# Kernel optimization log

Hardware: AMD Instinct MI355X
Metric: run time of the kernel (lower is better)

Reference implementation:

```python
import jax, jax.numpy as jnp
import numpy as np

N = 50000      # nodes
E = 800000     # edges (avg degree 16)
F_IN = 128     # num_features
HID = 128      # hidden_channels
C = 40         # num_classes


def setup_inputs() -> dict:
    key = jax.random.key(0)
    ks = jax.random.split(key, 8)
    x = jax.random.normal(ks[0], (N, F_IN), dtype=jnp.float32)
    edge_index = jax.random.randint(ks[1], (2, E), 0, N, dtype=jnp.int64)
    def glorot(k, fan_in, fan_out):
        s = np.sqrt(6.0 / (fan_in + fan_out)).astype(np.float32)
        return jax.random.uniform(k, (fan_in, fan_out), jnp.float32, -s, s)
    return {
        "x": x,
        "W1": glorot(ks[2], F_IN, HID), "b1": jnp.zeros((HID,), jnp.float32),
        "W2": glorot(ks[3], HID, HID),  "b2": jnp.zeros((HID,), jnp.float32),
        "W3": glorot(ks[4], HID, C),   "b3": jnp.zeros((C,), jnp.float32),
        "edge_index": edge_index,
    }


def reference(x, W1, b1, W2, b2, W3, b3, edge_index):
    # GCN with symmetric normalization and self-loops (PyG GCNConv semantics),
    # eval mode (dropout p=0.0), log-softmax output.
    src = edge_index[0]
    dst = edge_index[1]
    loop = jnp.arange(N, dtype=edge_index.dtype)
    src = jnp.concatenate([src, loop])      # [E+N]
    dst = jnp.concatenate([dst, loop])      # [E+N]
    ew = jnp.ones((E + N,), jnp.float32)    # edge_weight=None -> ones
    # deg[i] = sum of incoming edge weights at node i (aggregation index = dst/col)
    deg = jax.ops.segment_sum(ew, dst, num_segments=N)
    dinv = jnp.where(deg > 0, jax.lax.rsqrt(deg), 0.0)
    norm = dinv[src] * ew * dinv[dst]       # [E+N]

    def conv(h, W, b):
        # linear transform first (no bias), then gather->scale->scatter-add, then bias
        m = (h @ W)[src] * norm[:, None]                      # [E+N, out]
        return jax.ops.segment_sum(m, dst, num_segments=N) + b

    h = jax.nn.relu(conv(x, W1, b1))
    h = jax.nn.relu(conv(h, W2, b2))
    h = conv(h, W3, b3)
    return jax.nn.log_softmax(h, axis=-1)
```

## Files before the change

kernel.cpp:

```cpp
#include <hip/hip_runtime.h>
#include <math.h>

#define N_NODES 50000
#define N_EDGES 800000
#define BUCKET 64
#define SCAT_BLKS 196
#define GEMM_BLKS 196

typedef __attribute__((ext_vector_type(8))) short short8;
typedef __attribute__((ext_vector_type(4))) float f32x4;

__device__ __forceinline__ ushort f2bf(float f) {
    union { float f; uint u; } v; v.f = f;
    uint r = v.u + 0x7FFFu + ((v.u >> 16) & 1u);
    return (ushort)(r >> 16);
}
__device__ __forceinline__ float bflo(uint p) {
    union { uint u; float f; } v; v.u = p << 16; return v.f;
}
__device__ __forceinline__ float bfhi(uint p) {
    union { uint u; float f; } v; v.u = p & 0xFFFF0000u; return v.f;
}

__global__ __launch_bounds__(512) void fused_gemm1_scatter_k(
        const float* __restrict__ Af, const float* __restrict__ W, ushort* __restrict__ Y,
        const int* __restrict__ src, const int* __restrict__ dst,
        int* __restrict__ cnt, ushort* __restrict__ colb) {
    constexpr int NT = 8;
    __shared__ ushort sB[4 * NT * 64 * 8];
    const int tid = threadIdx.x;

    if (blockIdx.x < SCAT_BLKS) {
        const int t = blockIdx.x * 512 + tid;
        if (t >= N_EDGES / 8) return;
        const int4* s32 = reinterpret_cast<const int4*>(src);
        const int4* d32 = reinterpret_cast<const int4*>(dst);
        const int4 sa = s32[2 * t], sb = s32[2 * t + 1];
        const int4 da = d32[2 * t], db = d32[2 * t + 1];
        int p0 = atomicAdd(&cnt[da.x], 1);
        int p1 = atomicAdd(&cnt[da.y], 1);
        int p2 = atomicAdd(&cnt[da.z], 1);
        int p3 = atomicAdd(&cnt[da.w], 1);
        int p4 = atomicAdd(&cnt[db.x], 1);
        int p5 = atomicAdd(&cnt[db.y], 1);
        int p6 = atomicAdd(&cnt[db.z], 1);
        int p7 = atomicAdd(&cnt[db.w], 1);
        colb[(size_t)da.x * BUCKET + p0] = (ushort)sa.x;
        colb[(size_t)da.y * BUCKET + p1] = (ushort)sa.y;
        colb[(size_t)da.z * BUCKET + p2] = (ushort)sa.z;
        colb[(size_t)da.w * BUCKET + p3] = (ushort)sa.w;
        colb[(size_t)db.x * BUCKET + p4] = (ushort)sb.x;
        colb[(size_t)db.y * BUCKET + p5] = (ushort)sb.y;
        colb[(size_t)db.z * BUCKET + p6] = (ushort)sb.z;
        colb[(size_t)db.w * BUCKET + p7] = (ushort)sb.w;
        return;
    }

    constexpr int FP = NT * 16;
    for (int i = tid; i < 128 * FP; i += 512) {
        const int k = i / FP, n = i % FP;
        const int s = k >> 5, r2 = (k >> 3) & 3, j = k & 7;
        const int t = n >> 4, nl = n & 15;
        const int l = r2 * 16 + nl;
        const int lp = (l & 56) | ((l + (l >> 3)) & 7);
        sB[(((s * NT + t) * 64) + lp) * 8 + j] = f2bf(W[k * 128 + n]);
    }
    __syncthreads();

    const int wid = tid >> 6, lane = tid & 63;
    const int lp = (lane & 56) | ((lane + (lane >> 3)) & 7);
    const int t0 = (blockIdx.x - SCAT_BLKS) * 16 + wid * 2;
    const int t1 = t0 + 1;
    const int t0c = min(t0, N_NODES / 16 - 1);
    const int t1c = min(t1, N_NODES / 16 - 1);

    f32x4 acc[2][NT];
#pragma unroll
    for (int u = 0; u < 2; u++)
#pragma unroll
        for (int t = 0; t < NT; t++) acc[u][t] = (f32x4){0.f, 0.f, 0.f, 0.f};

#pragma unroll
    for (int s = 0; s < 4; s++) {
        short8 a0, a1;
        const int ko = 32 * s + 8 * (lane >> 4);
        const float4* p0 = reinterpret_cast<const float4*>(Af + (size_t)(t0c * 16 + (lane & 15)) * 128 + ko);
        const float4* p1 = reinterpret_cast<const float4*>(Af + (size_t)(t1c * 16 + (lane & 15)) * 128 + ko);
        float4 u0 = p0[0], u1 = p0[1], v0 = p1[0], v1 = p1[1];
        a0[0] = f2bf(u0.x); a0[1] = f2bf(u0.y); a0[2] = f2bf(u0.z); a0[3] = f2bf(u0.w);
        a0[4] = f2bf(u1.x); a0[5] = f2bf(u1.y); a0[6] = f2bf(u1.z); a0[7] = f2bf(u1.w);
        a1[0] = f2bf(v0.x); a1[1] = f2bf(v0.y); a1[2] = f2bf(v0.z); a1[3] = f2bf(v0.w);
        a1[4] = f2bf(v1.x); a1[5] = f2bf(v1.y); a1[6] = f2bf(v1.z); a1[7] = f2bf(v1.w);
#pragma unroll
        for (int t = 0; t < NT; t++) {
            short8 b = *reinterpret_cast<const short8*>(&sB[(((s * NT + t) * 64) + lp) * 8]);
            acc[0][t] = __builtin_amdgcn_mfma_f32_16x16x32_bf16(a0, b, acc[0][t], 0, 0, 0);
            acc[1][t] = __builtin_amdgcn_mfma_f32_16x16x32_bf16(a1, b, acc[1][t], 0, 0, 0);
        }
    }

    const int rl = 4 * (lane >> 4), cl = lane & 15;
#pragma unroll
    for (int u = 0; u < 2; u++) {
        const int tile = u ? t1 : t0;
        if (tile >= N_NODES / 16) continue;
        const int row0 = tile * 16;
#pragma unroll
        for (int t = 0; t < NT; t++) {
            const int c = 16 * t + cl;
#pragma unroll
            for (int g = 0; g < 4; g++)
                Y[(size_t)(row0 + rl + g) * 128 + c] = f2bf(acc[u][t][g]);
        }
    }
}

template <int NT>
__global__ __launch_bounds__(512) void gathergemm_k(const ushort* __restrict__ XW,
                                                    const int* __restrict__ cnt,
                                                    const ushort* __restrict__ colb,
                                                    const float* __restrict__ bias,
                                                    const float* __restrict__ W,
                                                    ushort* __restrict__ Y,
                                                    const int fout) {
    __shared__ ushort sB[4 * NT * 64 * 8];
    __shared__ uint sA[32 * 64];
    const int tid = threadIdx.x;
    const int wid = tid >> 6, lane = tid & 63;

    constexpr int FP = NT * 16;
    for (int i = tid; i < 128 * FP; i += 512) {
        const int k = i / FP, n = i % FP;
        const int s = k >> 5, r2 = (k >> 3) & 3, j = k & 7;
        const int t = n >> 4, nl = n & 15;
        const int l = r2 * 16 + nl;
        const int lpw = (l & 56) | ((l + (l >> 3)) & 7);
        sB[(((s * NT + t) * 64) + lpw) * 8 + j] = (n < fout) ? f2bf(W[k * fout + n]) : (ushort)0;
    }

    const int row0 = blockIdx.x * 32;
    const uint* XW32 = reinterpret_cast<const uint*>(XW);
#pragma unroll
    for (int u = 0; u < 4; u++) {
        const int r = wid * 4 + u;
        const int node = min(row0 + r, N_NODES - 1);
        const int n = cnt[node];
        const float di = rsqrtf((float)(n + 1));
        const ushort4* bucket = reinterpret_cast<const ushort4*>(colb + (size_t)node * BUCKET);

        float a0 = 0.f, a1 = 0.f, b0 = 0.f, b1 = 0.f;
        float c0 = 0.f, c1 = 0.f, d0 = 0.f, d1 = 0.f;
        int e = 0;
        for (; e + 4 <= n; e += 4) {
            const ushort4 s4 = bucket[e >> 2];
            const float w0 = rsqrtf((float)(cnt[s4.x] + 1)) * di;
            const float w1 = rsqrtf((float)(cnt[s4.y] + 1)) * di;
            const float w2 = rsqrtf((float)(cnt[s4.z] + 1)) * di;
            const float w3 = rsqrtf((float)(cnt[s4.w] + 1)) * di;
            const uint p0 = XW32[(size_t)s4.x * 64 + lane];
            const uint p1 = XW32[(size_t)s4.y * 64 + lane];
            const uint p2 = XW32[(size_t)s4.z * 64 + lane];
            const uint p3 = XW32[(size_t)s4.w * 64 + lane];
            a0 = fmaf(bflo(p0), w0, a0); a1 = fmaf(bfhi(p0), w0, a1);
            b0 = fmaf(bflo(p1), w1, b0); b1 = fmaf(bfhi(p1), w1, b1);
            c0 = fmaf(bflo(p2), w2, c0); c1 = fmaf(bfhi(p2), w2, c1);
            d0 = fmaf(bflo(p3), w3, d0); d1 = fmaf(bfhi(p3), w3, d1);
        }
        for (; e < n; e++) {
            const ushort s = colb[(size_t)node * BUCKET + e];
            const float w = rsqrtf((float)(cnt[s] + 1)) * di;
            const uint p = XW32[(size_t)s * 64 + lane];
            a0 = fmaf(bflo(p), w, a0); a1 = fmaf(bfhi(p), w, a1);
        }
        const uint ps = XW32[(size_t)node * 64 + lane];
        const float ws = di * di;
        a0 = fmaxf(fmaf(bflo(ps), ws, (a0 + b0) + (c0 + d0)) + bias[2 * lane], 0.f);
        a1 = fmaxf(fmaf(bfhi(ps), ws, (a1 + b1) + (c1 + d1)) + bias[2 * lane + 1], 0.f);
        sA[r * 64 + (lane ^ ((r & 7) << 2))] = (uint)f2bf(a0) | ((uint)f2bf(a1) << 16);
    }
    __syncthreads();

    if (NT == 3 && wid >= 6) return;
    const int tile = wid & 1;
    const int ar = tile * 16 + (lane & 15);
    const int hi = lane >> 4;
    const int lp = (lane & 56) | ((lane + (lane >> 3)) & 7);
    constexpr int UPW = (NT == 8) ? 2 : 1;

    f32x4 acc[UPW];
#pragma unroll
    for (int i = 0; i < UPW; i++) acc[i] = (f32x4){0.f, 0.f, 0.f, 0.f};

#pragma unroll
    for (int s = 0; s < 4; s++) {
        short8 a = *reinterpret_cast<const short8*>(
            &sA[ar * 64 + ((16 * s + 4 * hi) ^ ((ar & 7) << 2))]);
#pragma unroll
        for (int i = 0; i < UPW; i++) {
            const int t = (wid >> 1) + i * 4;
            short8 b = *reinterpret_cast<const short8*>(&sB[(((s * NT + t) * 64) + lp) * 8]);
            acc[i] = __builtin_amdgcn_mfma_f32_16x16x32_bf16(a, b, acc[i], 0, 0, 0);
        }
    }

    const int rl = 4 * hi, cl = lane & 15;
#pragma unroll
    for (int i = 0; i < UPW; i++) {
        const int t = (wid >> 1) + i * 4;
        const int c = 16 * t + cl;
        if (c >= fout) continue;
#pragma unroll
        for (int g = 0; g < 4; g++) {
            const int row = row0 + tile * 16 + rl + g;
            if (row < N_NODES) Y[(size_t)row * fout + c] = f2bf(acc[i][g]);
        }
    }
}

__global__ __launch_bounds__(256) void gather40_lsm_k(const ushort* __restrict__ XW,
                                                      const int* __restrict__ cnt,
                                                      const ushort* __restrict__ colb,
                                                      const float* __restrict__ bias,
                                                      float* __restrict__ out) {
    const int node = (blockIdx.x * 256 + threadIdx.x) >> 6;
    const int lane = threadIdx.x & 63;
    if (node >= N_NODES) return;
    const int g = lane < 20 ? 0 : (lane < 40 ? 1 : 2);
    const int ll = lane - g * 20;
    const int llc = min(ll, 19);
    const int n = cnt[node];
    const float di = rsqrtf((float)(n + 1));
    const uint* XW32 = reinterpret_cast<const uint*>(XW);

    float a0 = 0.f, a1 = 0.f;
    for (int e = g; e < n; e += 3) {
        const ushort s = colb[(size_t)node * BUCKET + e];
        const float w = rsqrtf((float)(cnt[s] + 1)) * di;
        const uint p = XW32[(size_t)s * 20 + llc];
        a0 = fmaf(bflo(p), w, a0); a1 = fmaf(bfhi(p), w, a1);
    }
    const float t1 = __shfl(a0, lane + 20), t2 = __shfl(a0, lane + 40);
    const float u1 = __shfl(a1, lane + 20), u2 = __shfl(a1, lane + 40);
    float v0 = -INFINITY, v1 = -INFINITY;
    if (lane < 20) {
        const float s0 = a0 + t1 + t2, s1 = a1 + u1 + u2;
        const uint ps = XW32[(size_t)node * 20 + lane];
        const float ws = di * di;
        v0 = fmaf(bflo(ps), ws, s0) + bias[2 * lane];
        v1 = fmaf(bfhi(ps), ws, s1) + bias[2 * lane + 1];
    }
    float m = fmaxf(v0, v1);
#pragma unroll
    for (int o = 32; o > 0; o >>= 1) m = fmaxf(m, __shfl_xor(m, o));
    float s = (lane < 20) ? (expf(v0 - m) + expf(v1 - m)) : 0.f;
#pragma unroll
    for (int o = 32; o > 0; o >>= 1) s += __shfl_xor(s, o);
    if (lane < 20) {
        const float ls = m + logf(s);
        float2 r; r.x = v0 - ls; r.y = v1 - ls;
        reinterpret_cast<float2*>(out)[(size_t)node * 20 + lane] = r;
    }
}

extern "C" void kernel_launch(void* const* d_in, const int* in_sizes, int n_in,
                              void* d_out, int out_size, void* d_ws, size_t ws_size,
                              hipStream_t stream) {
    const float* x  = (const float*)d_in[0];
    const float* W1 = (const float*)d_in[1];
    const float* b1 = (const float*)d_in[2];
    const float* W2 = (const float*)d_in[3];
    const float* b2 = (const float*)d_in[4];
    const float* W3 = (const float*)d_in[5];
    const float* b3 = (const float*)d_in[6];
    const int* ei   = (const int*)d_in[7];
    const int* srcp = ei;
    const int* dstp = ei + N_EDGES;
    float* out = (float*)d_out;

    int*    cnt  = (int*)d_ws;
    ushort* colb = (ushort*)(cnt + 50176);
    ushort* B0   = colb + (size_t)N_NODES * BUCKET;
    ushort* B1   = B0 + (size_t)N_NODES * 128;

    const int NB_W = (N_NODES * 64) / 256;
    const int NB_GG = (N_NODES + 31) / 32;

    hipMemsetAsync(cnt, 0, 50176 * sizeof(int), stream);
    fused_gemm1_scatter_k<<<SCAT_BLKS + GEMM_BLKS, 512, 0, stream>>>(
        x, W1, B1, srcp, dstp, cnt, colb);
    gathergemm_k<8><<<NB_GG, 512, 0, stream>>>(B1, cnt, colb, b1, W2, B0, 128);
    gathergemm_k<3><<<NB_GG, 512, 0, stream>>>(B0, cnt, colb, b2, W3, B1, 40);
    gather40_lsm_k<<<NB_W, 256, 0, stream>>>(B1, cnt, colb, b3, out);
}
```

Baseline: 287.5 us.

## Split gather-GEMM fusion into separate gather and row-prescaled GEMM kernels

Replaces the fused gather+GEMM kernels for layers 2 and 3 with standalone gather kernels and a GEMM that multiplies each output row by its source-degree normalization dinv. Later gathers can then sum neighbour rows without reading cnt per neighbour or calling rsqrt. The first gather loads neighbour indices and weights cooperatively across lanes and broadcasts them with shuffles. This adds two kernel launches and an extra round trip of intermediates through global memory, in exchange for cheaper inner gather loops and better GEMM occupancy.

```diff
diff --git a/kernel.cpp b/kernel.cpp
--- a/kernel.cpp
+++ b/kernel.cpp
@@ -116,108 +116,161 @@
 }
 
 template <int NT>
-__global__ __launch_bounds__(512) void gathergemm_k(const ushort* __restrict__ XW,
-                                                    const int* __restrict__ cnt,
-                                                    const ushort* __restrict__ colb,
-                                                    const float* __restrict__ bias,
-                                                    const float* __restrict__ W,
-                                                    ushort* __restrict__ Y,
-                                                    const int fout) {
+__global__ __launch_bounds__(512) void gemm_scaled_k(const ushort* __restrict__ Ab,
+                                                     const float* __restrict__ W,
+                                                     const int* __restrict__ cnt,
+                                                     ushort* __restrict__ Y,
+                                                     const int fout) {
     __shared__ ushort sB[4 * NT * 64 * 8];
-    __shared__ uint sA[32 * 64];
     const int tid = threadIdx.x;
-    const int wid = tid >> 6, lane = tid & 63;
-
     constexpr int FP = NT * 16;
     for (int i = tid; i < 128 * FP; i += 512) {
         const int k = i / FP, n = i % FP;
         const int s = k >> 5, r2 = (k >> 3) & 3, j = k & 7;
         const int t = n >> 4, nl = n & 15;
         const int l = r2 * 16 + nl;
-        const int lpw = (l & 56) | ((l + (l >> 3)) & 7);
-        sB[(((s * NT + t) * 64) + lpw) * 8 + j] = (n < fout) ? f2bf(W[k * fout + n]) : (ushort)0;
-    }
-
-    const int row0 = blockIdx.x * 32;
+        const int lp = (l & 56) | ((l + (l >> 3)) & 7);
+        sB[(((s * NT + t) * 64) + lp) * 8 + j] = (n < fout) ? f2bf(W[k * fout + n]) : (ushort)0;
+    }
+    __syncthreads();
+
+    const int wid = tid >> 6, lane = tid & 63;
+    const int lp = (lane & 56) | ((lane + (lane >> 3)) & 7);
+    const int t0 = blockIdx.x * 16 + wid * 2;
+    const int t1 = t0 + 1;
+    const int t0c = min(t0, N_NODES / 16 - 1);
+    const int t1c = min(t1, N_NODES / 16 - 1);
+
+    f32x4 acc[2][NT];
+#pragma unroll
+    for (int u = 0; u < 2; u++)
+#pragma unroll
+        for (int t = 0; t < NT; t++) acc[u][t] = (f32x4){0.f, 0.f, 0.f, 0.f};
+
+#pragma unroll
+    for (int s = 0; s < 4; s++) {
+        const int ko = 32 * s + 8 * (lane >> 4);
+        short8 a0 = *reinterpret_cast<const short8*>(Ab + (size_t)(t0c * 16 + (lane & 15)) * 128 + ko);
+        short8 a1 = *reinterpret_cast<const short8*>(Ab + (size_t)(t1c * 16 + (lane & 15)) * 128 + ko);
+#pragma unroll
+        for (int t = 0; t < NT; t++) {
+            short8 b = *reinterpret_cast<const short8*>(&sB[(((s * NT + t) * 64) + lp) * 8]);
+            acc[0][t] = __builtin_amdgcn_mfma_f32_16x16x32_bf16(a0, b, acc[0][t], 0, 0, 0);
+            acc[1][t] = __builtin_amdgcn_mfma_f32_16x16x32_bf16(a1, b, acc[1][t], 0, 0, 0);
+        }
+    }
+
+    const int rl = 4 * (lane >> 4), cl = lane & 15;
+#pragma unroll
+    for (int u = 0; u < 2; u++) {
+        const int tile = u ? t1 : t0;
+        if (tile >= N_NODES / 16) continue;
+        const int row0 = tile * 16;
+#pragma unroll
+        for (int g = 0; g < 4; g++) {
+            const int row = row0 + rl + g;
+            const float dr = rsqrtf((float)(cnt[row] + 1));
+#pragma unroll
+            for (int t = 0; t < NT; t++) {
+                const int c = 16 * t + cl;
+                if (NT == 3 && c >= fout) continue;
+                Y[(size_t)row * fout + c] = f2bf(acc[u][t][g] * dr);
+            }
+        }
+    }
+}
+
+__global__ __launch_bounds__(256) void gather1_k(const ushort* __restrict__ XW,
+                                                 const int* __restrict__ cnt,
+                                                 const ushort* __restrict__ colb,
+                                                 const float* __restrict__ bias,
+                                                 ushort* __restrict__ out) {
+    const int node = (blockIdx.x * 256 + threadIdx.x) >> 6;
+    const int lane = threadIdx.x & 63;
+    if (node >= N_NODES) return;
+    const int n = cnt[node];
+    const float di = rsqrtf((float)(n + 1));
+    int sl = 0; float wl = 0.f;
+    if (lane < n) {
+        sl = colb[(size_t)node * BUCKET + lane];
+        wl = rsqrtf((float)(cnt[sl] + 1));
+    }
     const uint* XW32 = reinterpret_cast<const uint*>(XW);
-#pragma unroll
-    for (int u = 0; u < 4; u++) {
-        const int r = wid * 4 + u;
-        const int node = min(row0 + r, N_NODES - 1);
-        const int n = cnt[node];
-        const float di = rsqrtf((float)(n + 1));
-        const ushort4* bucket = reinterpret_cast<const ushort4*>(colb + (size_t)node * BUCKET);
-
-        float a0 = 0.f, a1 = 0.f, b0 = 0.f, b1 = 0.f;
-        float c0 = 0.f, c1 = 0.f, d0 = 0.f, d1 = 0.f;
-        int e = 0;
-        for (; e + 4 <= n; e += 4) {
-            const ushort4 s4 = bucket[e >> 2];
-            const float w0 = rsqrtf((float)(cnt[s4.x] + 1)) * di;
-            const float w1 = rsqrtf((float)(cnt[s4.y] + 1)) * di;
-            const float w2 = rsqrtf((float)(cnt[s4.z] + 1)) * di;
-            const float w3 = rsqrtf((float)(cnt[s4.w] + 1)) * di;
-            const uint p0 = XW32[(size_t)s4.x * 64 + lane];
-            const uint p1 = XW32[(size_t)s4.y * 64 + lane];
-            const uint p2 = XW32[(size_t)s4.z * 64 + lane];
-            const uint p3 = XW32[(size_t)s4.w * 64 + lane];
-            a0 = fmaf(bflo(p0), w0, a0); a1 = fmaf(bfhi(p0), w0, a1);
-            b0 = fmaf(bflo(p1), w1, b0); b1 = fmaf(bfhi(p1), w1, b1);
-            c0 = fmaf(bflo(p2), w2, c0); c1 = fmaf(bfhi(p2), w2, c1);
-            d0 = fmaf(bflo(p3), w3, d0); d1 = fmaf(bfhi(p3), w3, d1);
-        }
-        for (; e < n; e++) {
-            const ushort s = colb[(size_t)node * BUCKET + e];
-            const float w = rsqrtf((float)(cnt[s] + 1)) * di;
-            const uint p = XW32[(size_t)s * 64 + lane];
-            a0 = fmaf(bflo(p), w, a0); a1 = fmaf(bfhi(p), w, a1);
-        }
-        const uint ps = XW32[(size_t)node * 64 + lane];
-        const float ws = di * di;
-        a0 = fmaxf(fmaf(bflo(ps), ws, (a0 + b0) + (c0 + d0)) + bias[2 * lane], 0.f);
-        a1 = fmaxf(fmaf(bfhi(ps), ws, (a1 + b1) + (c1 + d1)) + bias[2 * lane + 1], 0.f);
-        sA[r * 64 + (lane ^ ((r & 7) << 2))] = (uint)f2bf(a0) | ((uint)f2bf(a1) << 16);
-    }
-    __syncthreads();
-
-    if (NT == 3 && wid >= 6) return;
-    const int tile = wid & 1;
-    const int ar = tile * 16 + (lane & 15);
-    const int hi = lane >> 4;
-    const int lp = (lane & 56) | ((lane + (lane >> 3)) & 7);
-    constexpr int UPW = (NT == 8) ? 2 : 1;
-
-    f32x4 acc[UPW];
-#pragma unroll
-    for (int i = 0; i < UPW; i++) acc[i] = (f32x4){0.f, 0.f, 0.f, 0.f};
-
-#pragma unroll
-    for (int s = 0; s < 4; s++) {
-        short8 a = *reinterpret_cast<const short8*>(
-            &sA[ar * 64 + ((16 * s + 4 * hi) ^ ((ar & 7) << 2))]);
-#pragma unroll
-        for (int i = 0; i < UPW; i++) {
-            const int t = (wid >> 1) + i * 4;
-            short8 b = *reinterpret_cast<const short8*>(&sB[(((s * NT + t) * 64) + lp) * 8]);
-            acc[i] = __builtin_amdgcn_mfma_f32_16x16x32_bf16(a, b, acc[i], 0, 0, 0);
-        }
-    }
-
-    const int rl = 4 * hi, cl = lane & 15;
-#pragma unroll
-    for (int i = 0; i < UPW; i++) {
-        const int t = (wid >> 1) + i * 4;
-        const int c = 16 * t + cl;
-        if (c >= fout) continue;
-#pragma unroll
-        for (int g = 0; g < 4; g++) {
-            const int row = row0 + tile * 16 + rl + g;
-            if (row < N_NODES) Y[(size_t)row * fout + c] = f2bf(acc[i][g]);
-        }
-    }
-}
-
-__global__ __launch_bounds__(256) void gather40_lsm_k(const ushort* __restrict__ XW,
+
+    float a0 = 0.f, a1 = 0.f, b0 = 0.f, b1 = 0.f;
+    float c0 = 0.f, c1 = 0.f, d0 = 0.f, d1 = 0.f;
+    int e = 0;
+    for (; e + 4 <= n; e += 4) {
+        const int s0 = __shfl(sl, e),     s1 = __shfl(sl, e + 1);
+        const int s2 = __shfl(sl, e + 2), s3 = __shfl(sl, e + 3);
+        const float w0 = __shfl(wl, e),     w1 = __shfl(wl, e + 1);
+        const float w2 = __shfl(wl, e + 2), w3 = __shfl(wl, e + 3);
+        const uint p0 = XW32[(size_t)s0 * 64 + lane];
+        const uint p1 = XW32[(size_t)s1 * 64 + lane];
+        const uint p2 = XW32[(size_t)s2 * 64 + lane];
+        const uint p3 = XW32[(size_t)s3 * 64 + lane];
+        a0 = fmaf(bflo(p0), w0, a0); a1 = fmaf(bfhi(p0), w0, a1);
+        b0 = fmaf(bflo(p1), w1, b0); b1 = fmaf(bfhi(p1), w1, b1);
+        c0 = fmaf(bflo(p2), w2, c0); c1 = fmaf(bfhi(p2), w2, c1);
+        d0 = fmaf(bflo(p3), w3, d0); d1 = fmaf(bfhi(p3), w3, d1);
+    }
+    for (; e < n; e++) {
+        const int s = __shfl(sl, e);
+        const float w = __shfl(wl, e);
+        const uint p = XW32[(size_t)s * 64 + lane];
+        a0 = fmaf(bflo(p), w, a0); a1 = fmaf(bfhi(p), w, a1);
+    }
+    const uint ps = XW32[(size_t)node * 64 + lane];
+    float t0 = (a0 + b0) + (c0 + d0); t0 = fmaf(bflo(ps), di, t0);
+    float t1 = (a1 + b1) + (c1 + d1); t1 = fmaf(bfhi(ps), di, t1);
+    const float o0 = fmaxf(fmaf(di, t0, bias[2 * lane]), 0.f);
+    const float o1 = fmaxf(fmaf(di, t1, bias[2 * lane + 1]), 0.f);
+    reinterpret_cast<uint*>(out)[(size_t)node * 64 + lane] =
+        (uint)f2bf(o0) | ((uint)f2bf(o1) << 16);
+}
+
+__global__ __launch_bounds__(256) void gather_add_k(const ushort* __restrict__ XWn,
+                                                    const int* __restrict__ cnt,
+                                                    const ushort* __restrict__ colb,
+                                                    const float* __restrict__ bias,
+                                                    ushort* __restrict__ out) {
+    const int node = (blockIdx.x * 256 + threadIdx.x) >> 6;
+    const int lane = threadIdx.x & 63;
+    if (node >= N_NODES) return;
+    const int n = cnt[node];
+    const float di = rsqrtf((float)(n + 1));
+    const ushort4* bucket = reinterpret_cast<const ushort4*>(colb + (size_t)node * BUCKET);
+    const uint* XW32 = reinterpret_cast<const uint*>(XWn);
+
+    float a0 = 0.f, a1 = 0.f, b0 = 0.f, b1 = 0.f;
+    float c0 = 0.f, c1 = 0.f, d0 = 0.f, d1 = 0.f;
+    int e = 0;
+    for (; e + 4 <= n; e += 4) {
+        const ushort4 s4 = bucket[e >> 2];
+        const uint p0 = XW32[(size_t)s4.x * 64 + lane];
+        const uint p1 = XW32[(size_t)s4.y * 64 + lane];
+        const uint p2 = XW32[(size_t)s4.z * 64 + lane];
+        const uint p3 = XW32[(size_t)s4.w * 64 + lane];
+        a0 += bflo(p0); a1 += bfhi(p0);
+        b0 += bflo(p1); b1 += bfhi(p1);
+        c0 += bflo(p2); c1 += bfhi(p2);
+        d0 += bflo(p3); d1 += bfhi(p3);
+    }
+    for (; e < n; e++) {
+        const ushort s = colb[(size_t)node * BUCKET + e];
+        const uint p = XW32[(size_t)s * 64 + lane];
+        a0 += bflo(p); a1 += bfhi(p);
+    }
+    const uint ps = XW32[(size_t)node * 64 + lane];
+    const float t0 = ((a0 + b0) + (c0 + d0)) + bflo(ps);
+    const float t1 = ((a1 + b1) + (c1 + d1)) + bfhi(ps);
+    const float o0 = fmaxf(fmaf(di, t0, bias[2 * lane]), 0.f);
+    const float o1 = fmaxf(fmaf(di, t1, bias[2 * lane + 1]), 0.f);
+    reinterpret_cast<uint*>(out)[(size_t)node * 64 + lane] =
+        (uint)f2bf(o0) | ((uint)f2bf(o1) << 16);
+}
+
+__global__ __launch_bounds__(256) void gather40_lsm_k(const ushort* __restrict__ XWn,
                                                       const int* __restrict__ cnt,
                                                       const ushort* __restrict__ colb,
                                                       const float* __restrict__ bias,
@@ -230,24 +283,21 @@
     const int llc = min(ll, 19);
     const int n = cnt[node];
     const float di = rsqrtf((float)(n + 1));
-    const uint* XW32 = reinterpret_cast<const uint*>(XW);
+    const uint* XW32 = reinterpret_cast<const uint*>(XWn);
 
     float a0 = 0.f, a1 = 0.f;
     for (int e = g; e < n; e += 3) {
         const ushort s = colb[(size_t)node * BUCKET + e];
-        const float w = rsqrtf((float)(cnt[s] + 1)) * di;
         const uint p = XW32[(size_t)s * 20 + llc];
-        a0 = fmaf(bflo(p), w, a0); a1 = fmaf(bfhi(p), w, a1);
+        a0 += bflo(p); a1 += bfhi(p);
     }
     const float t1 = __shfl(a0, lane + 20), t2 = __shfl(a0, lane + 40);
     const float u1 = __shfl(a1, lane + 20), u2 = __shfl(a1, lane + 40);
     float v0 = -INFINITY, v1 = -INFINITY;
     if (lane < 20) {
-        const float s0 = a0 + t1 + t2, s1 = a1 + u1 + u2;
         const uint ps = XW32[(size_t)node * 20 + lane];
-        const float ws = di * di;
-        v0 = fmaf(bflo(ps), ws, s0) + bias[2 * lane];
-        v1 = fmaf(bfhi(ps), ws, s1) + bias[2 * lane + 1];
+        v0 = fmaf(di, (a0 + t1 + t2) + bflo(ps), bias[2 * lane]);
+        v1 = fmaf(di, (a1 + u1 + u2) + bfhi(ps), bias[2 * lane + 1]);
     }
     float m = fmaxf(v0, v1);
 #pragma unroll
@@ -283,12 +333,13 @@
     ushort* B1   = B0 + (size_t)N_NODES * 128;
 
     const int NB_W = (N_NODES * 64) / 256;
-    const int NB_GG = (N_NODES + 31) / 32;
 
     hipMemsetAsync(cnt, 0, 50176 * sizeof(int), stream);
     fused_gemm1_scatter_k<<<SCAT_BLKS + GEMM_BLKS, 512, 0, stream>>>(
         x, W1, B1, srcp, dstp, cnt, colb);
-    gathergemm_k<8><<<NB_GG, 512, 0, stream>>>(B1, cnt, colb, b1, W2, B0, 128);
-    gathergemm_k<3><<<NB_GG, 512, 0, stream>>>(B0, cnt, colb, b2, W3, B1, 40);
+    gather1_k<<<NB_W, 256, 0, stream>>>(B1, cnt, colb, b1, B0);
+    gemm_scaled_k<8><<<GEMM_BLKS, 512, 0, stream>>>(B0, W2, cnt, B1, 128);
+    gather_add_k<<<NB_W, 256, 0, stream>>>(B1, cnt, colb, b2, B0);
+    gemm_scaled_k<3><<<GEMM_BLKS, 512, 0, stream>>>(B0, W3, cnt, B1, 40);
     gather40_lsm_k<<<NB_W, 256, 0, stream>>>(B1, cnt, colb, b3, out);
 }
```

Measured after the change: 270.3 us. -6.0%, faster.
